# Kernel optimization log

Measured on AMD Instinct MI355X. Metric: run time of the kernel, lower is better.

The kernel has to match this reference:

```python
import jax, jax.numpy as jnp
import numpy as np

FILTERS = 256
KERNEL = 3
B, C, W = 8, 256, 8192
# he_std = gain / sqrt(fan_in) with fan_in = kernel_size * in_dim, lrmul = 1
RUNTIME_COEF = 1.0 / np.sqrt(KERNEL * C)


def setup_inputs() -> dict:
    key = jax.random.key(0)
    k1, k2, k3 = jax.random.split(key, 3)
    feature = jax.random.normal(k1, (B, C, W), dtype=jnp.float32)
    style = jax.random.normal(k2, (B, C), dtype=jnp.float32)
    kernel = jax.random.normal(k3, (KERNEL, C, FILTERS), dtype=jnp.float32)
    return {"feature": feature, "style": style, "kernel": kernel}


def reference(feature, style, kernel):
    b, c, w = feature.shape
    kk, _, f = kernel.shape
    # modulate: per-sample weights [B, k, C, F]
    weights = (kernel * RUNTIME_COEF)[None, ...] * (style[:, None, :, None] + 1.0)
    # demodulate: normalize over (k, C) per (B, F)
    denom = jax.lax.rsqrt(jnp.sum(jnp.square(weights), axis=(1, 2), keepdims=True))
    weights = weights * denom
    # batch-as-groups conv1d: lhs [1, B*C, W], rhs [k, C, B*F], groups = B
    lhs = feature.reshape(1, b * c, w)
    rhs = jnp.transpose(weights, (1, 2, 0, 3)).reshape(kk, c, b * f)
    out = jax.lax.conv_general_dilated(
        lhs, rhs,
        window_strides=(1,),
        padding="SAME",
        dimension_numbers=("NCH", "HIO", "NCH"),
        feature_group_count=b,
    )  # [1, B*F, W]
    return out.reshape(b, f, -1)
```

## Files before the change

### kernel.cpp

```cpp
#include <hip/hip_runtime.h>

#define B_   8
#define C_   256
#define W_   8192
#define F_   256
#define KK   3
#define KC   768
#define WP   (W_ + 2)
#define COEF 0.03608439182435161f
#define BK   64

using f32x16 = __attribute__((ext_vector_type(16))) float;
using bf16x8 = __attribute__((ext_vector_type(8))) __bf16;

#define AS1(p) ((const __attribute__((address_space(1))) void*)(p))
#define AS3(p) ((__attribute__((address_space(3))) void*)(p))

__device__ __forceinline__ unsigned short f2bf(float x) {
    union { float f; unsigned int u; } v; v.f = x;
    unsigned int u = v.u;
    u += 0x7FFFu + ((u >> 16) & 1u);
    return (unsigned short)(u >> 16);
}

__global__ void prep_kt(const float* __restrict__ kern, unsigned short* __restrict__ kT,
                        unsigned short* __restrict__ featT) {
    int idx = blockIdx.x * 256 + threadIdx.x;
    int f  = idx & 255;
    int kc = idx >> 8;
    kT[(size_t)f * KC + kc] = f2bf(kern[idx] * COEF);
    if (idx < 4096) {
        int b = idx >> 9, r = (idx >> 8) & 1, c = idx & 255;
        size_t row = r ? (size_t)(WP - 1) : 0;
        featT[((size_t)b * WP + row) * C_ + c] = 0;
    }
}

__global__ __launch_bounds__(256) void prep_denom(const float* __restrict__ kern,
                                                  const float* __restrict__ style,
                                                  float* __restrict__ denom) {
    __shared__ float sst[C_];
    const int b = blockIdx.x, f = threadIdx.x;
    sst[f] = (style[b * C_ + f] + 1.0f) * COEF;
    __syncthreads();
    float sum = 0.f;
#pragma unroll 8
    for (int kc = 0; kc < KC; ++kc) {
        float w = kern[(size_t)kc * F_ + f] * sst[kc & 255];
        sum += w * w;
    }
    denom[b * F_ + f] = rsqrtf(sum);
}

__global__ __launch_bounds__(256) void prep_featT(const float* __restrict__ feat,
                                                  const float* __restrict__ style,
                                                  unsigned short* __restrict__ featT) {
    __shared__ float tile[64][65];
    const int tid = threadIdx.x;
    const int b = blockIdx.z, c0 = blockIdx.y * 64, w0 = blockIdx.x * 64;

    const int x4 = tid & 15, cl4 = tid >> 4;
#pragma unroll
    for (int p = 0; p < 4; ++p) {
        const int cl = cl4 + p * 16;
        const float s = style[b * C_ + c0 + cl] + 1.0f;
        float4 v = *(const float4*)(feat + ((size_t)b * C_ + c0 + cl) * W_ + w0 + x4 * 4);
        tile[x4 * 4 + 0][cl] = v.x * s;
        tile[x4 * 4 + 1][cl] = v.y * s;
        tile[x4 * 4 + 2][cl] = v.z * s;
        tile[x4 * 4 + 3][cl] = v.w * s;
    }
    __syncthreads();

    const int ch = tid & 7, wr = tid >> 3;
#pragma unroll
    for (int p = 0; p < 2; ++p) {
        const int w = wr + p * 32;
        unsigned int pk[4];
#pragma unroll
        for (int j = 0; j < 4; ++j) {
            float v0 = tile[w][ch * 8 + 2 * j];
            float v1 = tile[w][ch * 8 + 2 * j + 1];
            pk[j] = (unsigned int)f2bf(v0) | ((unsigned int)f2bf(v1) << 16);
        }
        uint4 u; u.x = pk[0]; u.y = pk[1]; u.z = pk[2]; u.w = pk[3];
        *(uint4*)(featT + ((size_t)b * WP + (w0 + w + 1)) * C_ + c0 + ch * 8) = u;
    }
}

__global__ __launch_bounds__(256) void conv_mod(
        const unsigned short* __restrict__ featT,
        const unsigned short* __restrict__ kT,
        const float* __restrict__ denom,
        float* __restrict__ out) {
    __shared__ unsigned short As[128 * BK];
    __shared__ unsigned short Bs[128 * BK];

    const int tid  = threadIdx.x;
    const int b    = blockIdx.z;
    const int f0   = blockIdx.y * 128;
    const int w0   = blockIdx.x * 128;
    const int lane = tid & 63, wave = tid >> 6;
    const int wm   = (wave >> 1) * 64;
    const int wn   = (wave & 1) * 64;
    const int la   = lane & 31, kq = lane >> 5;

    const int lrow = lane >> 3, lchk = lane & 7, lswz = lchk ^ lrow;
    const unsigned short* asrc[4];
    const unsigned short* bsrc[4];
    int aldb[4], bldb[4];
#pragma unroll
    for (int i = 0; i < 4; ++i) {
        const int r = wave * 32 + i * 8;
        asrc[i] = kT + (size_t)(f0 + r + lrow) * KC + lswz * 8;
        bsrc[i] = featT + ((size_t)b * WP + (w0 + r + lrow)) * C_ + lswz * 8;
        aldb[i] = r * BK;
        bldb[i] = r * BK;
    }

    int aoff[2][4], boff[2][4];
#pragma unroll
    for (int mi = 0; mi < 2; ++mi) {
        const int row = wm + mi * 32 + la;
#pragma unroll
        for (int kh = 0; kh < 4; ++kh)
            aoff[mi][kh] = row * BK + ((kh * 2 + kq) ^ (la & 7)) * 8;
    }
#pragma unroll
    for (int ni = 0; ni < 2; ++ni) {
        const int row = wn + ni * 32 + la;
#pragma unroll
        for (int kh = 0; kh < 4; ++kh)
            boff[ni][kh] = row * BK + ((kh * 2 + kq) ^ (la & 7)) * 8;
    }

    f32x16 acc[2][2] = {};

    for (int it = 0; it < 12; ++it) {
        const int kc0 = it * 64;
        __syncthreads();
#pragma unroll
        for (int i = 0; i < 4; ++i) {
            __builtin_amdgcn_global_load_lds(AS1(asrc[i] + kc0), AS3(&As[aldb[i]]), 16, 0, 0);
            __builtin_amdgcn_global_load_lds(AS1(bsrc[i] + kc0), AS3(&Bs[bldb[i]]), 16, 0, 0);
        }
        __syncthreads();
#pragma unroll
        for (int kh = 0; kh < 4; ++kh) {
            bf16x8 a0 = *(const bf16x8*)&As[aoff[0][kh]];
            bf16x8 a1 = *(const bf16x8*)&As[aoff[1][kh]];
            bf16x8 b0 = *(const bf16x8*)&Bs[boff[0][kh]];
            bf16x8 b1 = *(const bf16x8*)&Bs[boff[1][kh]];
            acc[0][0] = __builtin_amdgcn_mfma_f32_32x32x16_bf16(a0, b0, acc[0][0], 0, 0, 0);
            acc[0][1] = __builtin_amdgcn_mfma_f32_32x32x16_bf16(a0, b1, acc[0][1], 0, 0, 0);
            acc[1][0] = __builtin_amdgcn_mfma_f32_32x32x16_bf16(a1, b0, acc[1][0], 0, 0, 0);
            acc[1][1] = __builtin_amdgcn_mfma_f32_32x32x16_bf16(a1, b1, acc[1][1], 0, 0, 0);
        }
    }

    const int bofs = b * F_;
    float* obase = out + (size_t)0;
#pragma unroll
    for (int mi = 0; mi < 2; ++mi) {
#pragma unroll
        for (int r = 0; r < 16; ++r) {
            const int frow = (r & 3) + 8 * (r >> 2) + 4 * kq;
            const int f = f0 + wm + mi * 32 + frow;
            const float d = denom[bofs + f];
            float* orow = obase + (size_t)(bofs + f) * W_ + w0 + wn + la;
            orow[0]  = acc[mi][0][r] * d;
            orow[32] = acc[mi][1][r] * d;
        }
    }
}

extern "C" void kernel_launch(void* const* d_in, const int* in_sizes, int n_in,
                              void* d_out, int out_size, void* d_ws, size_t ws_size,
                              hipStream_t stream) {
    const float* feature = (const float*)d_in[0];
    const float* style   = (const float*)d_in[1];
    const float* kern    = (const float*)d_in[2];
    float* out = (float*)d_out;

    unsigned short* kT    = (unsigned short*)d_ws;
    float*          denom = (float*)((char*)d_ws + (size_t)F_ * KC * 2);
    unsigned short* featT = (unsigned short*)((char*)d_ws + (size_t)F_ * KC * 2 + 8192);

    hipLaunchKernelGGL(prep_kt,    dim3(KC),     dim3(256), 0, stream, kern, kT, featT);
    hipLaunchKernelGGL(prep_denom, dim3(B_),     dim3(256), 0, stream, kern, style, denom);
    hipLaunchKernelGGL(prep_featT, dim3(W_ / 64, C_ / 64, B_), dim3(256), 0, stream,
                       feature, style, featT);
    hipLaunchKernelGGL(conv_mod,   dim3(W_ / 128, F_ / 128, B_), dim3(256), 0, stream,
                       featT, kT, denom, out);
}
```

Measured before the change: 177.5 us.

## Pipeline conv GEMM with triple-buffered LDS ring and full-F tiles; merge prep kernels

Restructures the conv GEMM so each block computes all 256 filters for a 128-wide W tile, using a 3-slot LDS ring with BK=32 and global_load_lds prefetch two stages ahead, synchronized by explicit vmcnt waits and barriers plus setprio around MFMA. This is meant to overlap global loads with MFMA compute and to stop featT being read twice, once per F-half. The two small prep kernels are merged into one launch to save launch overhead. It costs larger accumulators (4x2 32x32 tiles per wave), more register pressure, and half as many blocks in the grid.

Result: faster. 167.4 us (-5.7%).

```diff
diff --git a/kernel.cpp b/kernel.cpp
--- a/kernel.cpp
+++ b/kernel.cpp
@@ -8,7 +8,13 @@
 #define KC   768
 #define WP   (W_ + 2)
 #define COEF 0.03608439182435161f
-#define BK   64
+
+#define BN_   128
+#define BKc   32
+#define NT    24
+#define ASLOT 8192
+#define BSLOT 4096
+#define SLOT  12288
 
 using f32x16 = __attribute__((ext_vector_type(16))) float;
 using bf16x8 = __attribute__((ext_vector_type(8))) __bf16;
@@ -23,33 +29,33 @@
     return (unsigned short)(u >> 16);
 }
 
-__global__ void prep_kt(const float* __restrict__ kern, unsigned short* __restrict__ kT,
-                        unsigned short* __restrict__ featT) {
-    int idx = blockIdx.x * 256 + threadIdx.x;
-    int f  = idx & 255;
-    int kc = idx >> 8;
-    kT[(size_t)f * KC + kc] = f2bf(kern[idx] * COEF);
-    if (idx < 4096) {
-        int b = idx >> 9, r = (idx >> 8) & 1, c = idx & 255;
-        size_t row = r ? (size_t)(WP - 1) : 0;
-        featT[((size_t)b * WP + row) * C_ + c] = 0;
-    }
-}
-
-__global__ __launch_bounds__(256) void prep_denom(const float* __restrict__ kern,
-                                                  const float* __restrict__ style,
-                                                  float* __restrict__ denom) {
+__global__ __launch_bounds__(256) void prep_w(const float* __restrict__ kern,
+                                              const float* __restrict__ style,
+                                              unsigned short* __restrict__ kT,
+                                              float* __restrict__ denom,
+                                              unsigned short* __restrict__ featT) {
     __shared__ float sst[C_];
-    const int b = blockIdx.x, f = threadIdx.x;
-    sst[f] = (style[b * C_ + f] + 1.0f) * COEF;
-    __syncthreads();
-    float sum = 0.f;
-#pragma unroll 8
-    for (int kc = 0; kc < KC; ++kc) {
-        float w = kern[(size_t)kc * F_ + f] * sst[kc & 255];
-        sum += w * w;
-    }
-    denom[b * F_ + f] = rsqrtf(sum);
+    if (blockIdx.x < B_) {
+        const int b = blockIdx.x, f = threadIdx.x;
+        sst[f] = (style[b * C_ + f] + 1.0f) * COEF;
+        __syncthreads();
+        float sum = 0.f;
+#pragma unroll 16
+        for (int kc = 0; kc < KC; ++kc) {
+            float w = kern[(size_t)kc * F_ + f] * sst[kc & 255];
+            sum += w * w;
+        }
+        denom[b * F_ + f] = rsqrtf(sum);
+    } else {
+        const int idx = (blockIdx.x - B_) * 256 + threadIdx.x;
+        const int f = idx & 255, kc = idx >> 8;
+        kT[(size_t)f * KC + kc] = f2bf(kern[idx] * COEF);
+        if (idx < 4096) {
+            const int b = idx >> 9, r = (idx >> 8) & 1, c = idx & 255;
+            const size_t row = r ? (size_t)(WP - 1) : 0;
+            featT[((size_t)b * WP + row) * C_ + c] = 0;
+        }
+    }
 }
 
 __global__ __launch_bounds__(256) void prep_featT(const float* __restrict__ feat,
@@ -88,90 +94,144 @@
     }
 }
 
-__global__ __launch_bounds__(256) void conv_mod(
+__device__ __forceinline__ void compute_tile(const unsigned short* __restrict__ sb,
+                                             const int (&aoff)[4][2], const int (&boff)[2][2],
+                                             f32x16 (&acc)[4][2]) {
+    bf16x8 bf0 = *(const bf16x8*)&sb[boff[0][0]];
+    bf16x8 bf1 = *(const bf16x8*)&sb[boff[1][0]];
+    bf16x8 bg0 = *(const bf16x8*)&sb[boff[0][1]];
+    bf16x8 bg1 = *(const bf16x8*)&sb[boff[1][1]];
+#pragma unroll
+    for (int mi = 0; mi < 4; ++mi) {
+        bf16x8 a0 = *(const bf16x8*)&sb[aoff[mi][0]];
+        bf16x8 a1 = *(const bf16x8*)&sb[aoff[mi][1]];
+        acc[mi][0] = __builtin_amdgcn_mfma_f32_32x32x16_bf16(a0, bf0, acc[mi][0], 0, 0, 0);
+        acc[mi][1] = __builtin_amdgcn_mfma_f32_32x32x16_bf16(a0, bf1, acc[mi][1], 0, 0, 0);
+        acc[mi][0] = __builtin_amdgcn_mfma_f32_32x32x16_bf16(a1, bg0, acc[mi][0], 0, 0, 0);
+        acc[mi][1] = __builtin_amdgcn_mfma_f32_32x32x16_bf16(a1, bg1, acc[mi][1], 0, 0, 0);
+    }
+}
+
+__global__ __launch_bounds__(256, 2) void conv_mod(
         const unsigned short* __restrict__ featT,
         const unsigned short* __restrict__ kT,
         const float* __restrict__ denom,
         float* __restrict__ out) {
-    __shared__ unsigned short As[128 * BK];
-    __shared__ unsigned short Bs[128 * BK];
+    __shared__ __align__(16) unsigned short ring[3 * SLOT];
 
     const int tid  = threadIdx.x;
-    const int b    = blockIdx.z;
-    const int f0   = blockIdx.y * 128;
-    const int w0   = blockIdx.x * 128;
+    const int b    = blockIdx.y;
+    const int w0   = blockIdx.x * BN_;
     const int lane = tid & 63, wave = tid >> 6;
-    const int wm   = (wave >> 1) * 64;
+    const int wm   = (wave >> 1) * 128;
     const int wn   = (wave & 1) * 64;
     const int la   = lane & 31, kq = lane >> 5;
 
-    const int lrow = lane >> 3, lchk = lane & 7, lswz = lchk ^ lrow;
-    const unsigned short* asrc[4];
-    const unsigned short* bsrc[4];
-    int aldb[4], bldb[4];
-#pragma unroll
-    for (int i = 0; i < 4; ++i) {
-        const int r = wave * 32 + i * 8;
-        asrc[i] = kT + (size_t)(f0 + r + lrow) * KC + lswz * 8;
-        bsrc[i] = featT + ((size_t)b * WP + (w0 + r + lrow)) * C_ + lswz * 8;
-        aldb[i] = r * BK;
-        bldb[i] = r * BK;
-    }
-
-    int aoff[2][4], boff[2][4];
-#pragma unroll
-    for (int mi = 0; mi < 2; ++mi) {
+    const int lrow = lane >> 2, lswz = (lane & 3) ^ (lrow & 3);
+    const int r0 = wave * 16 + lrow;
+    const unsigned short* asrc0 = kT + (size_t)(r0)       * KC + lswz * 8;
+    const unsigned short* asrc1 = kT + (size_t)(r0 + 64)  * KC + lswz * 8;
+    const unsigned short* asrc2 = kT + (size_t)(r0 + 128) * KC + lswz * 8;
+    const unsigned short* asrc3 = kT + (size_t)(r0 + 192) * KC + lswz * 8;
+    const unsigned short* bsrc0 = featT + ((size_t)b * WP + (w0 + r0))      * C_ + lswz * 8;
+    const unsigned short* bsrc1 = featT + ((size_t)b * WP + (w0 + r0 + 64)) * C_ + lswz * 8;
+    const int al0 = (wave * 16)       * BKc;
+    const int al1 = (wave * 16 + 64)  * BKc;
+    const int al2 = (wave * 16 + 128) * BKc;
+    const int al3 = (wave * 16 + 192) * BKc;
+    const int bl0 = ASLOT + (wave * 16)      * BKc;
+    const int bl1 = ASLOT + (wave * 16 + 64) * BKc;
+
+    int aoff[4][2], boff[2][2];
+#pragma unroll
+    for (int mi = 0; mi < 4; ++mi) {
         const int row = wm + mi * 32 + la;
 #pragma unroll
-        for (int kh = 0; kh < 4; ++kh)
-            aoff[mi][kh] = row * BK + ((kh * 2 + kq) ^ (la & 7)) * 8;
+        for (int kh = 0; kh < 2; ++kh)
+            aoff[mi][kh] = row * BKc + (((kh * 2 + kq) ^ (la & 3)) * 8);
     }
 #pragma unroll
     for (int ni = 0; ni < 2; ++ni) {
         const int row = wn + ni * 32 + la;
 #pragma unroll
-        for (int kh = 0; kh < 4; ++kh)
-            boff[ni][kh] = row * BK + ((kh * 2 + kq) ^ (la & 7)) * 8;
-    }
-
-    f32x16 acc[2][2] = {};
-
-    for (int it = 0; it < 12; ++it) {
-        const int kc0 = it * 64;
-        __syncthreads();
-#pragma unroll
-        for (int i = 0; i < 4; ++i) {
-            __builtin_amdgcn_global_load_lds(AS1(asrc[i] + kc0), AS3(&As[aldb[i]]), 16, 0, 0);
-            __builtin_amdgcn_global_load_lds(AS1(bsrc[i] + kc0), AS3(&Bs[bldb[i]]), 16, 0, 0);
-        }
-        __syncthreads();
-#pragma unroll
-        for (int kh = 0; kh < 4; ++kh) {
-            bf16x8 a0 = *(const bf16x8*)&As[aoff[0][kh]];
-            bf16x8 a1 = *(const bf16x8*)&As[aoff[1][kh]];
-            bf16x8 b0 = *(const bf16x8*)&Bs[boff[0][kh]];
-            bf16x8 b1 = *(const bf16x8*)&Bs[boff[1][kh]];
-            acc[0][0] = __builtin_amdgcn_mfma_f32_32x32x16_bf16(a0, b0, acc[0][0], 0, 0, 0);
-            acc[0][1] = __builtin_amdgcn_mfma_f32_32x32x16_bf16(a0, b1, acc[0][1], 0, 0, 0);
-            acc[1][0] = __builtin_amdgcn_mfma_f32_32x32x16_bf16(a1, b0, acc[1][0], 0, 0, 0);
-            acc[1][1] = __builtin_amdgcn_mfma_f32_32x32x16_bf16(a1, b1, acc[1][1], 0, 0, 0);
-        }
-    }
+        for (int kh = 0; kh < 2; ++kh)
+            boff[ni][kh] = ASLOT + row * BKc + (((kh * 2 + kq) ^ (la & 3)) * 8);
+    }
+
+#define STAGE(t, s) do { \
+        const int ko = (t) * BKc; \
+        unsigned short* rs = &ring[(s) * SLOT]; \
+        __builtin_amdgcn_global_load_lds(AS1(asrc0 + ko), AS3(rs + al0), 16, 0, 0); \
+        __builtin_amdgcn_global_load_lds(AS1(asrc1 + ko), AS3(rs + al1), 16, 0, 0); \
+        __builtin_amdgcn_global_load_lds(AS1(asrc2 + ko), AS3(rs + al2), 16, 0, 0); \
+        __builtin_amdgcn_global_load_lds(AS1(asrc3 + ko), AS3(rs + al3), 16, 0, 0); \
+        __builtin_amdgcn_global_load_lds(AS1(bsrc0 + ko), AS3(rs + bl0), 16, 0, 0); \
+        __builtin_amdgcn_global_load_lds(AS1(bsrc1 + ko), AS3(rs + bl1), 16, 0, 0); \
+    } while (0)
+
+#define ITER_END(N) do { \
+        __builtin_amdgcn_sched_barrier(0); \
+        asm volatile("s_waitcnt vmcnt(" #N ")" ::: "memory"); \
+        __builtin_amdgcn_s_barrier(); \
+        asm volatile("" ::: "memory"); \
+    } while (0)
+
+    f32x16 acc[4][2] = {};
+
+    STAGE(0, 0);
+    STAGE(1, 1);
+    asm volatile("s_waitcnt vmcnt(6)" ::: "memory");
+    __builtin_amdgcn_s_barrier();
+    asm volatile("" ::: "memory");
+
+#pragma unroll 1
+    for (int j = 0; j < 7; ++j) {
+        const int t = j * 3;
+        STAGE(t + 2, 2);
+        __builtin_amdgcn_s_setprio(1);
+        compute_tile(&ring[0], aoff, boff, acc);
+        __builtin_amdgcn_s_setprio(0);
+        ITER_END(6);
+        STAGE(t + 3, 0);
+        __builtin_amdgcn_s_setprio(1);
+        compute_tile(&ring[SLOT], aoff, boff, acc);
+        __builtin_amdgcn_s_setprio(0);
+        ITER_END(6);
+        STAGE(t + 4, 1);
+        __builtin_amdgcn_s_setprio(1);
+        compute_tile(&ring[2 * SLOT], aoff, boff, acc);
+        __builtin_amdgcn_s_setprio(0);
+        ITER_END(6);
+    }
+    STAGE(23, 2);
+    __builtin_amdgcn_s_setprio(1);
+    compute_tile(&ring[0], aoff, boff, acc);
+    __builtin_amdgcn_s_setprio(0);
+    ITER_END(6);
+    __builtin_amdgcn_s_setprio(1);
+    compute_tile(&ring[SLOT], aoff, boff, acc);
+    __builtin_amdgcn_s_setprio(0);
+    ITER_END(0);
+    __builtin_amdgcn_s_setprio(1);
+    compute_tile(&ring[2 * SLOT], aoff, boff, acc);
+    __builtin_amdgcn_s_setprio(0);
 
     const int bofs = b * F_;
-    float* obase = out + (size_t)0;
-#pragma unroll
-    for (int mi = 0; mi < 2; ++mi) {
+    float* obase = out + (size_t)bofs * W_ + w0;
+#pragma unroll
+    for (int mi = 0; mi < 4; ++mi) {
 #pragma unroll
         for (int r = 0; r < 16; ++r) {
             const int frow = (r & 3) + 8 * (r >> 2) + 4 * kq;
-            const int f = f0 + wm + mi * 32 + frow;
+            const int f = wm + mi * 32 + frow;
             const float d = denom[bofs + f];
-            float* orow = obase + (size_t)(bofs + f) * W_ + w0 + wn + la;
+            float* orow = obase + (size_t)f * W_ + wn + la;
             orow[0]  = acc[mi][0][r] * d;
             orow[32] = acc[mi][1][r] * d;
         }
     }
+#undef STAGE
+#undef ITER_END
 }
 
 extern "C" void kernel_launch(void* const* d_in, const int* in_sizes, int n_in,
@@ -186,10 +246,10 @@
     float*          denom = (float*)((char*)d_ws + (size_t)F_ * KC * 2);
     unsigned short* featT = (unsigned short*)((char*)d_ws + (size_t)F_ * KC * 2 + 8192);
 
-    hipLaunchKernelGGL(prep_kt,    dim3(KC),     dim3(256), 0, stream, kern, kT, featT);
-    hipLaunchKernelGGL(prep_denom, dim3(B_),     dim3(256), 0, stream, kern, style, denom);
+    hipLaunchKernelGGL(prep_w,     dim3(KC + B_), dim3(256), 0, stream,
+                       kern, style, kT, denom, featT);
     hipLaunchKernelGGL(prep_featT, dim3(W_ / 64, C_ / 64, B_), dim3(256), 0, stream,
                        feature, style, featT);
-    hipLaunchKernelGGL(conv_mod,   dim3(W_ / 128, F_ / 128, B_), dim3(256), 0, stream,
+    hipLaunchKernelGGL(conv_mod,   dim3(W_ / BN_, B_), dim3(256), 0, stream,
                        featT, kT, denom, out);
 }
```

## Double-buffer conv GEMM with 256x256 tiles, phased prefetch, and merged prep kernels

Applied to the files above, without the earlier changes.

The conv GEMM now uses 512-thread blocks covering all 256 filters by 256 width positions, with a double-buffered LDS ring. Global-to-LDS loads for the next K slice are issued in the middle of the MFMA phases, gated by explicit vmcnt waits and barriers, with setprio raised around the MFMAs. This is meant to hide load latency and cut repeated reads of featT. The two small weight-prep kernels are merged into one launch to drop launch overhead. The larger tile doubles the LDS footprint and register pressure, and there are fewer blocks in the grid.

New measurement: 170.3 us. 1.04x faster.

```diff
diff --git a/kernel.cpp b/kernel.cpp
--- a/kernel.cpp
+++ b/kernel.cpp
@@ -8,7 +8,13 @@
 #define KC   768
 #define WP   (W_ + 2)
 #define COEF 0.03608439182435161f
-#define BK   64
+
+#define BN_   256
+#define BKc   64
+#define NT    12
+#define ABASE 0
+#define BBASE 16384
+#define BUFU  32768
 
 using f32x16 = __attribute__((ext_vector_type(16))) float;
 using bf16x8 = __attribute__((ext_vector_type(8))) __bf16;
@@ -23,33 +29,33 @@
     return (unsigned short)(u >> 16);
 }
 
-__global__ void prep_kt(const float* __restrict__ kern, unsigned short* __restrict__ kT,
-                        unsigned short* __restrict__ featT) {
-    int idx = blockIdx.x * 256 + threadIdx.x;
-    int f  = idx & 255;
-    int kc = idx >> 8;
-    kT[(size_t)f * KC + kc] = f2bf(kern[idx] * COEF);
-    if (idx < 4096) {
-        int b = idx >> 9, r = (idx >> 8) & 1, c = idx & 255;
-        size_t row = r ? (size_t)(WP - 1) : 0;
-        featT[((size_t)b * WP + row) * C_ + c] = 0;
-    }
-}
-
-__global__ __launch_bounds__(256) void prep_denom(const float* __restrict__ kern,
-                                                  const float* __restrict__ style,
-                                                  float* __restrict__ denom) {
+__global__ __launch_bounds__(256) void prep_w(const float* __restrict__ kern,
+                                              const float* __restrict__ style,
+                                              unsigned short* __restrict__ kT,
+                                              float* __restrict__ denom,
+                                              unsigned short* __restrict__ featT) {
     __shared__ float sst[C_];
-    const int b = blockIdx.x, f = threadIdx.x;
-    sst[f] = (style[b * C_ + f] + 1.0f) * COEF;
-    __syncthreads();
-    float sum = 0.f;
-#pragma unroll 8
-    for (int kc = 0; kc < KC; ++kc) {
-        float w = kern[(size_t)kc * F_ + f] * sst[kc & 255];
-        sum += w * w;
-    }
-    denom[b * F_ + f] = rsqrtf(sum);
+    if (blockIdx.x < B_) {
+        const int b = blockIdx.x, f = threadIdx.x;
+        sst[f] = (style[b * C_ + f] + 1.0f) * COEF;
+        __syncthreads();
+        float sum = 0.f;
+#pragma unroll 16
+        for (int kc = 0; kc < KC; ++kc) {
+            float w = kern[(size_t)kc * F_ + f] * sst[kc & 255];
+            sum += w * w;
+        }
+        denom[b * F_ + f] = rsqrtf(sum);
+    } else {
+        const int idx = (blockIdx.x - B_) * 256 + threadIdx.x;
+        const int f = idx & 255, kc = idx >> 8;
+        kT[(size_t)f * KC + kc] = f2bf(kern[idx] * COEF);
+        if (idx < 4096) {
+            const int b = idx >> 9, r = (idx >> 8) & 1, c = idx & 255;
+            const size_t row = r ? (size_t)(WP - 1) : 0;
+            featT[((size_t)b * WP + row) * C_ + c] = 0;
+        }
+    }
 }
 
 __global__ __launch_bounds__(256) void prep_featT(const float* __restrict__ feat,
@@ -88,90 +94,123 @@
     }
 }
 
-__global__ __launch_bounds__(256) void conv_mod(
+__global__ __launch_bounds__(512, 2) void conv_mod(
         const unsigned short* __restrict__ featT,
         const unsigned short* __restrict__ kT,
         const float* __restrict__ denom,
         float* __restrict__ out) {
-    __shared__ unsigned short As[128 * BK];
-    __shared__ unsigned short Bs[128 * BK];
+    __shared__ __align__(16) unsigned short ring[2 * BUFU];
 
     const int tid  = threadIdx.x;
-    const int b    = blockIdx.z;
-    const int f0   = blockIdx.y * 128;
-    const int w0   = blockIdx.x * 128;
+    const int b    = blockIdx.y;
+    const int w0   = blockIdx.x * BN_;
     const int lane = tid & 63, wave = tid >> 6;
-    const int wm   = (wave >> 1) * 64;
-    const int wn   = (wave & 1) * 64;
+    const int wm   = (wave >> 2) * 128;
+    const int wn   = (wave & 3) * 64;
     const int la   = lane & 31, kq = lane >> 5;
 
-    const int lrow = lane >> 3, lchk = lane & 7, lswz = lchk ^ lrow;
-    const unsigned short* asrc[4];
-    const unsigned short* bsrc[4];
-    int aldb[4], bldb[4];
-#pragma unroll
-    for (int i = 0; i < 4; ++i) {
-        const int r = wave * 32 + i * 8;
-        asrc[i] = kT + (size_t)(f0 + r + lrow) * KC + lswz * 8;
-        bsrc[i] = featT + ((size_t)b * WP + (w0 + r + lrow)) * C_ + lswz * 8;
-        aldb[i] = r * BK;
-        bldb[i] = r * BK;
-    }
-
-    int aoff[2][4], boff[2][4];
-#pragma unroll
-    for (int mi = 0; mi < 2; ++mi) {
-        const int row = wm + mi * 32 + la;
-#pragma unroll
-        for (int kh = 0; kh < 4; ++kh)
-            aoff[mi][kh] = row * BK + ((kh * 2 + kq) ^ (la & 7)) * 8;
-    }
-#pragma unroll
-    for (int ni = 0; ni < 2; ++ni) {
-        const int row = wn + ni * 32 + la;
-#pragma unroll
-        for (int kh = 0; kh < 4; ++kh)
-            boff[ni][kh] = row * BK + ((kh * 2 + kq) ^ (la & 7)) * 8;
-    }
-
-    f32x16 acc[2][2] = {};
-
-    for (int it = 0; it < 12; ++it) {
-        const int kc0 = it * 64;
-        __syncthreads();
-#pragma unroll
-        for (int i = 0; i < 4; ++i) {
-            __builtin_amdgcn_global_load_lds(AS1(asrc[i] + kc0), AS3(&As[aldb[i]]), 16, 0, 0);
-            __builtin_amdgcn_global_load_lds(AS1(bsrc[i] + kc0), AS3(&Bs[bldb[i]]), 16, 0, 0);
-        }
-        __syncthreads();
-#pragma unroll
-        for (int kh = 0; kh < 4; ++kh) {
-            bf16x8 a0 = *(const bf16x8*)&As[aoff[0][kh]];
-            bf16x8 a1 = *(const bf16x8*)&As[aoff[1][kh]];
-            bf16x8 b0 = *(const bf16x8*)&Bs[boff[0][kh]];
-            bf16x8 b1 = *(const bf16x8*)&Bs[boff[1][kh]];
-            acc[0][0] = __builtin_amdgcn_mfma_f32_32x32x16_bf16(a0, b0, acc[0][0], 0, 0, 0);
-            acc[0][1] = __builtin_amdgcn_mfma_f32_32x32x16_bf16(a0, b1, acc[0][1], 0, 0, 0);
-            acc[1][0] = __builtin_amdgcn_mfma_f32_32x32x16_bf16(a1, b0, acc[1][0], 0, 0, 0);
-            acc[1][1] = __builtin_amdgcn_mfma_f32_32x32x16_bf16(a1, b1, acc[1][1], 0, 0, 0);
-        }
-    }
+    const int srow = tid >> 3;
+    const int sswz = ((tid & 7) ^ (srow & 7)) * 8;
+    const unsigned short* aS0 = kT + (size_t)srow * KC + sswz;
+    const unsigned short* bS0 = featT + ((size_t)b * WP + w0 + srow) * C_ + sswz;
+    const int wdst = wave << 9;
+
+    int ck[4];
+#pragma unroll
+    for (int kh = 0; kh < 4; ++kh) ck[kh] = ((kh * 2 + kq) ^ (la & 7)) * 8;
+    const int ra = (wm + la) * BKc;
+    const int rb = BBASE + (wn + la) * BKc;
+
+    f32x16 acc[4][2] = {};
+
+#define GLDS_A(g, kc, nb) __builtin_amdgcn_global_load_lds( \
+        AS1(aS0 + (size_t)(g) * 64 * KC + (kc)), \
+        AS3((nb) + ABASE + (g) * 4096 + wdst), 16, 0, 0)
+#define GLDS_B(g, kc, nb) __builtin_amdgcn_global_load_lds( \
+        AS1(bS0 + (size_t)(g) * 64 * C_ + (kc)), \
+        AS3((nb) + BBASE + (g) * 4096 + wdst), 16, 0, 0)
+#define PH_BAR() do { __builtin_amdgcn_s_barrier(); \
+                      asm volatile("" ::: "memory"); } while (0)
+#define VMW(n) do { __builtin_amdgcn_sched_barrier(0); \
+                    asm volatile("s_waitcnt vmcnt(" #n ")" ::: "memory"); } while (0)
+
+#define PHASE(MH, KH2) do { \
+        bf16x8 av[2][2], bv[2][2]; \
+        _Pragma("unroll") \
+        for (int i = 0; i < 2; ++i) { \
+            _Pragma("unroll") \
+            for (int j = 0; j < 2; ++j) { \
+                av[i][j] = *(const bf16x8*)&bf[ra + ((MH) * 2 + i) * 2048 + ck[(KH2) * 2 + j]]; \
+                bv[i][j] = *(const bf16x8*)&bf[rb + i * 2048 + ck[(KH2) * 2 + j]]; \
+            } \
+        } \
+        __builtin_amdgcn_s_setprio(1); \
+        _Pragma("unroll") \
+        for (int j = 0; j < 2; ++j) { \
+            _Pragma("unroll") \
+            for (int i = 0; i < 2; ++i) { \
+                acc[(MH) * 2 + i][0] = __builtin_amdgcn_mfma_f32_32x32x16_bf16(av[i][j], bv[0][j], acc[(MH) * 2 + i][0], 0, 0, 0); \
+                acc[(MH) * 2 + i][1] = __builtin_amdgcn_mfma_f32_32x32x16_bf16(av[i][j], bv[1][j], acc[(MH) * 2 + i][1], 0, 0, 0); \
+            } \
+        } \
+        __builtin_amdgcn_s_setprio(0); \
+    } while (0)
+
+    {
+        unsigned short* nb = ring;
+        GLDS_A(0, 0, nb); GLDS_A(2, 0, nb);
+        GLDS_B(0, 0, nb); GLDS_B(1, 0, nb);
+        GLDS_B(2, 0, nb); GLDS_B(3, 0, nb);
+        GLDS_A(1, 0, nb); GLDS_A(3, 0, nb);
+    }
+    VMW(2);
+    PH_BAR();
+
+#pragma unroll 1
+    for (int t = 0; t < NT; ++t) {
+        const unsigned short* bf = ring + (t & 1) * BUFU;
+        unsigned short* nb = ring + ((t + 1) & 1) * BUFU;
+        const int kn = (t < NT - 1 ? t + 1 : NT - 1) * BKc;
+
+        GLDS_A(0, kn, nb); GLDS_A(2, kn, nb);
+        GLDS_B(0, kn, nb); GLDS_B(1, kn, nb);
+        PHASE(0, 0);
+        PH_BAR();
+
+        GLDS_B(2, kn, nb); GLDS_B(3, kn, nb);
+        GLDS_A(1, kn, nb); GLDS_A(3, kn, nb);
+        PHASE(0, 1);
+        VMW(8);
+        PH_BAR();
+
+        PHASE(1, 0);
+        PH_BAR();
+
+        PHASE(1, 1);
+        VMW(2);
+        PH_BAR();
+    }
+    asm volatile("s_waitcnt vmcnt(0)" ::: "memory");
 
     const int bofs = b * F_;
-    float* obase = out + (size_t)0;
-#pragma unroll
-    for (int mi = 0; mi < 2; ++mi) {
+    float* obase = out + (size_t)bofs * W_ + w0;
+#pragma unroll
+    for (int mi = 0; mi < 4; ++mi) {
 #pragma unroll
         for (int r = 0; r < 16; ++r) {
             const int frow = (r & 3) + 8 * (r >> 2) + 4 * kq;
-            const int f = f0 + wm + mi * 32 + frow;
+            const int f = wm + mi * 32 + frow;
             const float d = denom[bofs + f];
-            float* orow = obase + (size_t)(bofs + f) * W_ + w0 + wn + la;
+            float* orow = obase + (size_t)f * W_ + wn + la;
             orow[0]  = acc[mi][0][r] * d;
             orow[32] = acc[mi][1][r] * d;
         }
     }
+#undef GLDS_A
+#undef GLDS_B
+#undef PH_BAR
+#undef VMW
+#undef PHASE
 }
 
 extern "C" void kernel_launch(void* const* d_in, const int* in_sizes, int n_in,
@@ -186,10 +225,10 @@
     float*          denom = (float*)((char*)d_ws + (size_t)F_ * KC * 2);
     unsigned short* featT = (unsigned short*)((char*)d_ws + (size_t)F_ * KC * 2 + 8192);
 
-    hipLaunchKernelGGL(prep_kt,    dim3(KC),     dim3(256), 0, stream, kern, kT, featT);
-    hipLaunchKernelGGL(prep_denom, dim3(B_),     dim3(256), 0, stream, kern, style, denom);
+    hipLaunchKernelGGL(prep_w,     dim3(KC + B_), dim3(256), 0, stream,
+                       kern, style, kT, denom, featT);
     hipLaunchKernelGGL(prep_featT, dim3(W_ / 64, C_ / 64, B_), dim3(256), 0, stream,
                        feature, style, featT);
-    hipLaunchKernelGGL(conv_mod,   dim3(W_ / 128, F_ / 128, B_), dim3(256), 0, stream,
+    hipLaunchKernelGGL(conv_mod,   dim3(W_ / BN_, B_), dim3(512), 0, stream,
                        featT, kT, denom, out);
 }
```
